# Performance work log

Measured on AMD Instinct MI355X. Metric: run time of the kernel, lower is better.

## Reference

```python
import jax, jax.numpy as jnp
import numpy as np

ALPHA = 0.2  # leaky_relu negative slope
NEG_INF = -9e15


def gat_layer(h_in, W, a, adj_mask):
    """One GATLayer (eval mode, dropout disabled).
    h_in: [N, F_in], W: [F_in, F_out], a: [2*F_out, 1], adj_mask: [N, N] bool.
    Equivalent to the torch repeat/cat construction: e_ij = leaky_relu(a1.h_i + a2.h_j).
    """
    h = h_in @ W                          # [N, F_out]
    F_out = W.shape[1]
    a1 = a[:F_out, 0]                     # [F_out]
    a2 = a[F_out:, 0]                     # [F_out]
    f1 = h @ a1                           # [N]
    f2 = h @ a2                           # [N]
    e = jax.nn.leaky_relu(f1[:, None] + f2[None, :], negative_slope=ALPHA)  # [N, N]
    e = jnp.where(adj_mask, e, NEG_INF)
    attn = jax.nn.softmax(e, axis=-1)     # rows sum to 1
    return jax.nn.elu(attn @ h)           # [N, F_out]


def setup_inputs() -> dict:
    key = jax.random.key(0)
    ks = jax.random.split(key, 6)
    N, F_in, F_hid, F_out, H = 8192, 29, 8, 2, 4
    x = jax.random.normal(ks[0], (N, F_in), dtype=jnp.float32)
    adj = jax.random.randint(ks[1], (N, N), 0, 2, dtype=jnp.int32)
    # xavier_uniform with gain=1.414
    def xavier(k, shape, gain=1.414):
        fan_in, fan_out = shape[0], shape[1]
        bound = gain * np.sqrt(6.0 / (fan_in + fan_out))
        return jax.random.uniform(k, shape, jnp.float32, -bound, bound)
    W_heads = jnp.stack([xavier(k, (F_in, F_hid)) for k in jax.random.split(ks[2], H)])   # [H, 29, 8]
    a_heads = jnp.stack([xavier(k, (2 * F_hid, 1)) for k in jax.random.split(ks[3], H)])  # [H, 16, 1]
    W_out = xavier(ks[4], (F_hid * H, F_out))   # [32, 2]
    a_out = xavier(ks[5], (2 * F_out, 1))       # [4, 1]
    return {"x": x, "adj": adj, "W_heads": W_heads, "a_heads": a_heads,
            "W_out": W_out, "a_out": a_out}


def reference(x, adj, W_heads, a_heads, W_out, a_out):
    adj_mask = adj > 0
    heads = jax.vmap(lambda W, a: gat_layer(x, W, a, adj_mask))(W_heads, a_heads)  # [H, N, 8]
    hcat = jnp.concatenate(list(heads), axis=1)   # [N, H*8] (same order as torch cat over heads)
    out = gat_layer(hcat, W_out, a_out, adj_mask)  # [N, 2]
    return jax.nn.log_softmax(out, axis=1)
```

## Files before the change

kernel.cpp:

```cpp
#include <hip/hip_runtime.h>
#include <math.h>

#define N 8192
#define NW 128
#define FIN 29
#define FH 8
#define NH 4
#define ALPHA 0.2f
#define LOG2E 1.4426950408889634f

typedef unsigned long long ull;

__device__ inline unsigned bf16rn(float f) {
    unsigned u = __float_as_uint(f);
    return (u + 0x7fffu + ((u >> 16) & 1u)) >> 16;
}
__device__ inline float2 bfpair(unsigned u) {
    return make_float2(__uint_as_float(u << 16), __uint_as_float(u & 0xffff0000u));
}
__device__ inline unsigned fenc(float x) {
    unsigned u = __float_as_uint(x);
    return (u & 0x80000000u) ? ~u : (u | 0x80000000u);
}
__device__ inline float fdec(unsigned e) {
    return __uint_as_float((e & 0x80000000u) ? (e & 0x7fffffffu) : ~e);
}

__global__ void k0_pack(const int* __restrict__ adj, ull* __restrict__ mask,
                        unsigned* __restrict__ amax) {
    int row = blockIdx.x;
    int tid = threadIdx.x;
    int lane = tid & 63;
    int wave = tid >> 6;
    if (row == 0 && tid < 8) amax[tid] = 0u;
    const int* rp = adj + (size_t)row * N;
#pragma unroll 8
    for (int i = 0; i < 32; i++) {
        int a = rp[i * 256 + tid];
        ull b = __ballot(a > 0);
        if (lane == 0) mask[(size_t)row * NW + i * 4 + wave] = b;
    }
}

__global__ __launch_bounds__(64) void k1_feat(
    const float* __restrict__ x, const float* __restrict__ Wh,
    const float* __restrict__ ah,
    float* __restrict__ f2p, uint4* __restrict__ hpk,
    float* __restrict__ f1a, unsigned* __restrict__ amax) {
    __shared__ float sW[NH * FIN * FH];
    __shared__ float sa[NH * 2 * FH];
    int tid = threadIdx.x;
    for (int i = tid; i < NH * FIN * FH; i += 64) sW[i] = Wh[i];
    for (int i = tid; i < NH * 2 * FH; i += 64) sa[i] = ah[i];
    __syncthreads();
    int node = blockIdx.x * 64 + tid;
    float xr[FIN];
#pragma unroll
    for (int f = 0; f < FIN; f++) xr[f] = x[node * FIN + f];
    float f2v[NH];
#pragma unroll
    for (int h = 0; h < NH; h++) {
        float hv[FH];
#pragma unroll
        for (int k = 0; k < FH; k++) {
            float s = 0.f;
#pragma unroll
            for (int f = 0; f < FIN; f++) s += xr[f] * sW[(h * FIN + f) * FH + k];
            hv[k] = s;
        }
        float f1 = 0.f, f2 = 0.f;
#pragma unroll
        for (int k = 0; k < FH; k++) {
            f1 += hv[k] * sa[h * 16 + k];
            f2 += hv[k] * sa[h * 16 + 8 + k];
        }
        f2v[h] = f2 * LOG2E;
        f2p[h * N + node] = f2v[h];
        f1a[node * 4 + h] = f1 * LOG2E;
        uint4 p;
        p.x = (bf16rn(hv[1]) << 16) | bf16rn(hv[0]);
        p.y = (bf16rn(hv[3]) << 16) | bf16rn(hv[2]);
        p.z = (bf16rn(hv[5]) << 16) | bf16rn(hv[4]);
        p.w = (bf16rn(hv[7]) << 16) | bf16rn(hv[6]);
        hpk[h * N + node] = p;
    }
#pragma unroll
    for (int h = 0; h < NH; h++) {
        float v = f2v[h];
        for (int off = 32; off > 0; off >>= 1) v = fmaxf(v, __shfl_xor(v, off, 64));
        if (tid == 0) atomicMax(&amax[h], fenc(v));
    }
}

#define TJ 512
#define JS1 2
__global__ __launch_bounds__(512) void k3_attn1(
    const ull* __restrict__ mask, const float* __restrict__ f2p,
    const uint4* __restrict__ hpk, const float* __restrict__ f1a,
    const unsigned* __restrict__ amax, float* __restrict__ part1) {
    __shared__ float tF2[TJ];
    __shared__ uint4 tH[TJ];
    int tid = threadIdx.x;
    int lane = tid & 63;
    int wave = tid >> 6;
    int h = blockIdx.x & 3;
    int js = (blockIdx.x >> 2) & (JS1 - 1);
    int rowblk = blockIdx.x >> 3;
    int r0 = rowblk * 16 + wave * 2;
    int r1 = r0 + 1;
    const int JR = N / JS1;
    int jbase = js * JR;

    float mf = fdec(amax[h]);
    float f1 = f1a[r0 * 4 + h];
    float v = f1 + mf, m = fmaxf(v, ALPHA * v);
    float f1m0 = f1 - m, f1q0 = ALPHA * f1 - m;
    f1 = f1a[r1 * 4 + h];
    v = f1 + mf; m = fmaxf(v, ALPHA * v);
    float f1m1 = f1 - m, f1q1 = ALPHA * f1 - m;

    float acc0[FH], acc1[FH], d0 = 0.f, d1 = 0.f;
#pragma unroll
    for (int k = 0; k < FH; k++) { acc0[k] = 0.f; acc1[k] = 0.f; }

    const ull* mr0 = mask + (size_t)r0 * NW;
    const ull* mr1 = mask + (size_t)r1 * NW;

    for (int t = 0; t < JR / TJ; t++) {
        __syncthreads();
        int gb = jbase + t * TJ + tid;
        tH[tid] = hpk[h * N + gb];
        tF2[tid] = f2p[h * N + gb];
        __syncthreads();
        int wb = (jbase >> 6) + t * (TJ / 64);
#pragma unroll
        for (int s = 0; s < TJ / 64; s++) {
            ull mw0 = mr0[wb + s];
            ull mw1 = mr1[wb + s];
            bool b0 = (mw0 >> lane) & 1ull;
            bool b1 = (mw1 >> lane) & 1ull;
            int jl = s * 64 + lane;
            float f2 = tF2[jl];
            uint4 hq = tH[jl];
            float2 hv01 = bfpair(hq.x);
            float2 hv23 = bfpair(hq.y);
            float2 hv45 = bfpair(hq.z);
            float2 hv67 = bfpair(hq.w);
            float p = ALPHA * f2;
            float w0 = __builtin_amdgcn_exp2f(fmaxf(f1m0 + f2, p + f1q0));
            w0 = b0 ? w0 : 0.f;
            float w1 = __builtin_amdgcn_exp2f(fmaxf(f1m1 + f2, p + f1q1));
            w1 = b1 ? w1 : 0.f;
            acc0[0] = fmaf(w0, hv01.x, acc0[0]);
            acc0[1] = fmaf(w0, hv01.y, acc0[1]);
            acc0[2] = fmaf(w0, hv23.x, acc0[2]);
            acc0[3] = fmaf(w0, hv23.y, acc0[3]);
            acc0[4] = fmaf(w0, hv45.x, acc0[4]);
            acc0[5] = fmaf(w0, hv45.y, acc0[5]);
            acc0[6] = fmaf(w0, hv67.x, acc0[6]);
            acc0[7] = fmaf(w0, hv67.y, acc0[7]);
            d0 += w0;
            acc1[0] = fmaf(w1, hv01.x, acc1[0]);
            acc1[1] = fmaf(w1, hv01.y, acc1[1]);
            acc1[2] = fmaf(w1, hv23.x, acc1[2]);
            acc1[3] = fmaf(w1, hv23.y, acc1[3]);
            acc1[4] = fmaf(w1, hv45.x, acc1[4]);
            acc1[5] = fmaf(w1, hv45.y, acc1[5]);
            acc1[6] = fmaf(w1, hv67.x, acc1[6]);
            acc1[7] = fmaf(w1, hv67.y, acc1[7]);
            d1 += w1;
        }
    }
#pragma unroll
    for (int k = 0; k < FH; k++) {
        for (int off = 32; off > 0; off >>= 1) {
            acc0[k] += __shfl_xor(acc0[k], off, 64);
            acc1[k] += __shfl_xor(acc1[k], off, 64);
        }
    }
    for (int off = 32; off > 0; off >>= 1) {
        d0 += __shfl_xor(d0, off, 64);
        d1 += __shfl_xor(d1, off, 64);
    }
    if (lane == 0) {
#pragma unroll
        for (int k = 0; k < FH; k++) {
            part1[(js * 36 + h * 9 + k) * N + r0] = acc0[k];
            part1[(js * 36 + h * 9 + k) * N + r1] = acc1[k];
        }
        part1[(js * 36 + h * 9 + 8) * N + r0] = d0;
        part1[(js * 36 + h * 9 + 8) * N + r1] = d1;
    }
}

__global__ void k3b_final(const float* __restrict__ part1, const float* __restrict__ Wo,
                          const float* __restrict__ ao,
                          float4* __restrict__ rec2, float* __restrict__ f1b,
                          unsigned* __restrict__ amax) {
    __shared__ float sW[64];
    __shared__ float sa[4];
    int tid = threadIdx.x;
    if (tid < 64) sW[tid] = Wo[tid];
    if (tid < 4) sa[tid] = ao[tid];
    __syncthreads();
    int row = blockIdx.x * 256 + tid;
    float hv[32];
#pragma unroll
    for (int h = 0; h < NH; h++) {
        float s[9];
#pragma unroll
        for (int c = 0; c < 9; c++)
            s[c] = part1[(h * 9 + c) * N + row] + part1[(36 + h * 9 + c) * N + row];
        float inv = 1.f / s[8];
#pragma unroll
        for (int k = 0; k < FH; k++) {
            float o = s[k] * inv;
            hv[h * 8 + k] = (o > 0.f) ? o : expm1f(o);
        }
    }
    float h0 = 0.f, h1 = 0.f;
#pragma unroll
    for (int i = 0; i < 32; i++) {
        h0 = fmaf(hv[i], sW[i * 2 + 0], h0);
        h1 = fmaf(hv[i], sW[i * 2 + 1], h1);
    }
    float f1 = (h0 * sa[0] + h1 * sa[1]) * LOG2E;
    float f2 = (h0 * sa[2] + h1 * sa[3]) * LOG2E;
    rec2[row] = make_float4(f2, h0, h1, 0.f);
    f1b[row] = f1;
    float vmax = f2;
    for (int off = 32; off > 0; off >>= 1) vmax = fmaxf(vmax, __shfl_xor(vmax, off, 64));
    if ((tid & 63) == 0) atomicMax(&amax[4], fenc(vmax));
}

#define JS2 4
__global__ __launch_bounds__(256) void k6_attn2(
    const ull* __restrict__ mask, const float4* __restrict__ rec2,
    const float* __restrict__ f1b, const unsigned* __restrict__ amax,
    float* __restrict__ part2) {
    int tid = threadIdx.x;
    int lane = tid & 63;
    int wave = tid >> 6;
    int blk = blockIdx.x >> 2;
    int js = blockIdx.x & 3;
    int rbase = blk * 16 + wave * 4;
    const int JR = N / JS2;
    int jbase = js * JR;

    float mb = fdec(amax[4]);
    float f1m[4], f1q[4];
#pragma unroll
    for (int i = 0; i < 4; i++) {
        float f1 = f1b[rbase + i];
        float v = f1 + mb, m = fmaxf(v, ALPHA * v);
        f1m[i] = f1 - m; f1q[i] = ALPHA * f1 - m;
    }
    float a0[4] = {0.f, 0.f, 0.f, 0.f};
    float a1[4] = {0.f, 0.f, 0.f, 0.f};
    float dd[4] = {0.f, 0.f, 0.f, 0.f};
    const ull* mr[4];
#pragma unroll
    for (int i = 0; i < 4; i++) mr[i] = mask + (size_t)(rbase + i) * NW;

    int wb = jbase >> 6;
#pragma unroll 4
    for (int s = 0; s < JR / 64; s++) {
        float4 q = rec2[jbase + s * 64 + lane];
        float p = ALPHA * q.x;
#pragma unroll
        for (int i = 0; i < 4; i++) {
            ull mw = mr[i][wb + s];
            float w = __builtin_amdgcn_exp2f(fmaxf(f1m[i] + q.x, p + f1q[i]));
            w = ((mw >> lane) & 1ull) ? w : 0.f;
            a0[i] = fmaf(w, q.y, a0[i]);
            a1[i] = fmaf(w, q.z, a1[i]);
            dd[i] += w;
        }
    }
#pragma unroll
    for (int i = 0; i < 4; i++) {
        for (int off = 32; off > 0; off >>= 1) {
            a0[i] += __shfl_xor(a0[i], off, 64);
            a1[i] += __shfl_xor(a1[i], off, 64);
            dd[i] += __shfl_xor(dd[i], off, 64);
        }
    }
    if (lane == 0) {
#pragma unroll
        for (int i = 0; i < 4; i++) {
            int row = rbase + i;
            part2[(js * 3 + 0) * N + row] = a0[i];
            part2[(js * 3 + 1) * N + row] = a1[i];
            part2[(js * 3 + 2) * N + row] = dd[i];
        }
    }
}

__global__ void k6b_final(const float* __restrict__ part2, float* __restrict__ out) {
    int row = blockIdx.x * 256 + threadIdx.x;
    float s0 = 0.f, s1 = 0.f, d = 0.f;
#pragma unroll
    for (int js = 0; js < JS2; js++) {
        s0 += part2[(js * 3 + 0) * N + row];
        s1 += part2[(js * 3 + 1) * N + row];
        d  += part2[(js * 3 + 2) * N + row];
    }
    float inv = 1.f / d;
    float e0 = s0 * inv, e1 = s1 * inv;
    e0 = (e0 > 0.f) ? e0 : expm1f(e0);
    e1 = (e1 > 0.f) ? e1 : expm1f(e1);
    float mx = fmaxf(e0, e1);
    float lse = mx + logf(expf(e0 - mx) + expf(e1 - mx));
    ((float2*)out)[row] = make_float2(e0 - lse, e1 - lse);
}

extern "C" void kernel_launch(void* const* d_in, const int* in_sizes, int n_in,
                              void* d_out, int out_size, void* d_ws, size_t ws_size,
                              hipStream_t stream) {
    const float* x   = (const float*)d_in[0];
    const int*   adj = (const int*)d_in[1];
    const float* Wh  = (const float*)d_in[2];
    const float* ah  = (const float*)d_in[3];
    const float* Wo  = (const float*)d_in[4];
    const float* ao  = (const float*)d_in[5];
    float* out = (float*)d_out;
    float* ws = (float*)d_ws;

    ull*      mask  = (ull*)ws;
    float*    f2p   = ws + 2097152;
    uint4*    hpk   = (uint4*)(ws + 2129920);
    float*    f1a   = ws + 2260992;
    float*    part1 = ws + 2293760;
    float4*   rec2  = (float4*)(ws + 2883584);
    float*    f1b   = ws + 2916352;
    float*    part2 = ws + 2924544;
    unsigned* amax  = (unsigned*)(ws + 3022848);

    k0_pack<<<N, 256, 0, stream>>>(adj, mask, amax);
    k1_feat<<<N / 64, 64, 0, stream>>>(x, Wh, ah, f2p, hpk, f1a, amax);
    k3_attn1<<<(N / 16) * JS1 * NH, 512, 0, stream>>>(mask, f2p, hpk, f1a, amax, part1);
    k3b_final<<<N / 256, 256, 0, stream>>>(part1, Wo, ao, rec2, f1b, amax);
    k6_attn2<<<(N / 16) * JS2, 256, 0, stream>>>(mask, rec2, f1b, amax, part2);
    k6b_final<<<N / 256, 256, 0, stream>>>(part2, out);
}
```

Baseline: 617.6 us.

## Compute first-layer attention aggregation with bf16 MFMA and factored exponentials

```diff
diff --git a/kernel.cpp b/kernel.cpp
--- a/kernel.cpp
+++ b/kernel.cpp
@@ -8,15 +8,18 @@
 #define NH 4
 #define ALPHA 0.2f
 #define LOG2E 1.4426950408889634f
+#define JS 4
+#define JRR (N / JS)
+#define JS2 4
 
 typedef unsigned long long ull;
+typedef unsigned short u16;
+typedef __attribute__((ext_vector_type(8))) short bf16x8;
+typedef __attribute__((ext_vector_type(4))) float f32x4;
 
 __device__ inline unsigned bf16rn(float f) {
     unsigned u = __float_as_uint(f);
     return (u + 0x7fffu + ((u >> 16) & 1u)) >> 16;
-}
-__device__ inline float2 bfpair(unsigned u) {
-    return make_float2(__uint_as_float(u << 16), __uint_as_float(u & 0xffff0000u));
 }
 __device__ inline unsigned fenc(float x) {
     unsigned u = __float_as_uint(x);
@@ -45,7 +48,7 @@
 __global__ __launch_bounds__(64) void k1_feat(
     const float* __restrict__ x, const float* __restrict__ Wh,
     const float* __restrict__ ah,
-    float* __restrict__ f2p, uint4* __restrict__ hpk,
+    float2* __restrict__ e2, u16* __restrict__ Ht,
     float* __restrict__ f1a, unsigned* __restrict__ amax) {
     __shared__ float sW[NH * FIN * FH];
     __shared__ float sa[NH * 2 * FH];
@@ -74,15 +77,15 @@
             f1 += hv[k] * sa[h * 16 + k];
             f2 += hv[k] * sa[h * 16 + 8 + k];
         }
-        f2v[h] = f2 * LOG2E;
-        f2p[h * N + node] = f2v[h];
-        f1a[node * 4 + h] = f1 * LOG2E;
-        uint4 p;
-        p.x = (bf16rn(hv[1]) << 16) | bf16rn(hv[0]);
-        p.y = (bf16rn(hv[3]) << 16) | bf16rn(hv[2]);
-        p.z = (bf16rn(hv[5]) << 16) | bf16rn(hv[4]);
-        p.w = (bf16rn(hv[7]) << 16) | bf16rn(hv[6]);
-        hpk[h * N + node] = p;
+        float f1L = f1 * LOG2E, f2L = f2 * LOG2E;
+        f2v[h] = f2L;
+        f1a[node * 4 + h] = f1L;
+        e2[h * N + node] = make_float2(__builtin_amdgcn_exp2f(f2L),
+                                       __builtin_amdgcn_exp2f(ALPHA * f2L));
+#pragma unroll
+        for (int k = 0; k < FH; k++)
+            Ht[(size_t)(h * 9 + k) * N + node] = (u16)bf16rn(hv[k]);
+        Ht[(size_t)(h * 9 + 8) * N + node] = 0x3F80u;
     }
 #pragma unroll
     for (int h = 0; h < NH; h++) {
@@ -92,104 +95,84 @@
     }
 }
 
-#define TJ 512
-#define JS1 2
-__global__ __launch_bounds__(512) void k3_attn1(
-    const ull* __restrict__ mask, const float* __restrict__ f2p,
-    const uint4* __restrict__ hpk, const float* __restrict__ f1a,
+__global__ __launch_bounds__(256) void k3_attn1(
+    const ull* __restrict__ mask, const float2* __restrict__ e2,
+    const u16* __restrict__ Ht, const float* __restrict__ f1a,
     const unsigned* __restrict__ amax, float* __restrict__ part1) {
-    __shared__ float tF2[TJ];
-    __shared__ uint4 tH[TJ];
+    __shared__ __align__(16) float2 sE2[JRR];
     int tid = threadIdx.x;
     int lane = tid & 63;
     int wave = tid >> 6;
     int h = blockIdx.x & 3;
-    int js = (blockIdx.x >> 2) & (JS1 - 1);
-    int rowblk = blockIdx.x >> 3;
-    int r0 = rowblk * 16 + wave * 2;
-    int r1 = r0 + 1;
-    const int JR = N / JS1;
-    int jbase = js * JR;
-
-    float mf = fdec(amax[h]);
-    float f1 = f1a[r0 * 4 + h];
-    float v = f1 + mf, m = fmaxf(v, ALPHA * v);
-    float f1m0 = f1 - m, f1q0 = ALPHA * f1 - m;
-    f1 = f1a[r1 * 4 + h];
-    v = f1 + mf; m = fmaxf(v, ALPHA * v);
-    float f1m1 = f1 - m, f1q1 = ALPHA * f1 - m;
-
-    float acc0[FH], acc1[FH], d0 = 0.f, d1 = 0.f;
-#pragma unroll
-    for (int k = 0; k < FH; k++) { acc0[k] = 0.f; acc1[k] = 0.f; }
-
-    const ull* mr0 = mask + (size_t)r0 * NW;
-    const ull* mr1 = mask + (size_t)r1 * NW;
-
-    for (int t = 0; t < JR / TJ; t++) {
-        __syncthreads();
-        int gb = jbase + t * TJ + tid;
-        tH[tid] = hpk[h * N + gb];
-        tF2[tid] = f2p[h * N + gb];
-        __syncthreads();
-        int wb = (jbase >> 6) + t * (TJ / 64);
-#pragma unroll
-        for (int s = 0; s < TJ / 64; s++) {
-            ull mw0 = mr0[wb + s];
-            ull mw1 = mr1[wb + s];
-            bool b0 = (mw0 >> lane) & 1ull;
-            bool b1 = (mw1 >> lane) & 1ull;
-            int jl = s * 64 + lane;
-            float f2 = tF2[jl];
-            uint4 hq = tH[jl];
-            float2 hv01 = bfpair(hq.x);
-            float2 hv23 = bfpair(hq.y);
-            float2 hv45 = bfpair(hq.z);
-            float2 hv67 = bfpair(hq.w);
-            float p = ALPHA * f2;
-            float w0 = __builtin_amdgcn_exp2f(fmaxf(f1m0 + f2, p + f1q0));
-            w0 = b0 ? w0 : 0.f;
-            float w1 = __builtin_amdgcn_exp2f(fmaxf(f1m1 + f2, p + f1q1));
-            w1 = b1 ? w1 : 0.f;
-            acc0[0] = fmaf(w0, hv01.x, acc0[0]);
-            acc0[1] = fmaf(w0, hv01.y, acc0[1]);
-            acc0[2] = fmaf(w0, hv23.x, acc0[2]);
-            acc0[3] = fmaf(w0, hv23.y, acc0[3]);
-            acc0[4] = fmaf(w0, hv45.x, acc0[4]);
-            acc0[5] = fmaf(w0, hv45.y, acc0[5]);
-            acc0[6] = fmaf(w0, hv67.x, acc0[6]);
-            acc0[7] = fmaf(w0, hv67.y, acc0[7]);
-            d0 += w0;
-            acc1[0] = fmaf(w1, hv01.x, acc1[0]);
-            acc1[1] = fmaf(w1, hv01.y, acc1[1]);
-            acc1[2] = fmaf(w1, hv23.x, acc1[2]);
-            acc1[3] = fmaf(w1, hv23.y, acc1[3]);
-            acc1[4] = fmaf(w1, hv45.x, acc1[4]);
-            acc1[5] = fmaf(w1, hv45.y, acc1[5]);
-            acc1[6] = fmaf(w1, hv67.x, acc1[6]);
-            acc1[7] = fmaf(w1, hv67.y, acc1[7]);
-            d1 += w1;
-        }
-    }
-#pragma unroll
-    for (int k = 0; k < FH; k++) {
-        for (int off = 32; off > 0; off >>= 1) {
-            acc0[k] += __shfl_xor(acc0[k], off, 64);
-            acc1[k] += __shfl_xor(acc1[k], off, 64);
-        }
-    }
-    for (int off = 32; off > 0; off >>= 1) {
-        d0 += __shfl_xor(d0, off, 64);
-        d1 += __shfl_xor(d1, off, 64);
-    }
-    if (lane == 0) {
-#pragma unroll
-        for (int k = 0; k < FH; k++) {
-            part1[(js * 36 + h * 9 + k) * N + r0] = acc0[k];
-            part1[(js * 36 + h * 9 + k) * N + r1] = acc1[k];
-        }
-        part1[(js * 36 + h * 9 + 8) * N + r0] = d0;
-        part1[(js * 36 + h * 9 + 8) * N + r1] = d1;
+    int js = (blockIdx.x >> 2) & 3;
+    int rowblk = blockIdx.x >> 4;
+    int jbase = js * JRR;
+
+    {
+        const float4* src = (const float4*)(e2 + (size_t)h * N + jbase);
+        float4* dst = (float4*)sE2;
+#pragma unroll
+        for (int i = 0; i < (JRR / 2) / 256; i++)
+            dst[tid + i * 256] = src[tid + i * 256];
+    }
+
+    int c = lane & 15;
+    int kb = lane >> 4;
+    int sh = kb * 8;
+    int r = rowblk * 64 + wave * 16 + c;
+
+    float mfL = fdec(amax[h]);
+    float f1 = f1a[r * 4 + h];
+    float v = f1 + mfL, m = fmaxf(v, ALPHA * v);
+    float e1p = __builtin_amdgcn_exp2f(f1 - m);
+    float e1n = __builtin_amdgcn_exp2f(ALPHA * f1 - m);
+
+    const ull* mrow = mask + (size_t)r * NW + (jbase >> 6);
+    const char* bbase = (const char*)(Ht + ((size_t)(h * 9 + c) * N + jbase + kb * 8));
+
+    f32x4 acc = {0.f, 0.f, 0.f, 0.f};
+    __syncthreads();
+
+    for (int t = 0; t < JRR / 64; t++) {
+        ull mw = mrow[t];
+        unsigned mlo = (unsigned)mw;
+        unsigned mhi = (unsigned)(mw >> 32);
+#pragma unroll
+        for (int hf = 0; hf < 2; hf++) {
+            unsigned sw = (hf ? mhi : mlo) >> sh;
+            const float4* qp = (const float4*)(sE2 + t * 64 + hf * 32 + kb * 8);
+            float4 q0 = qp[0], q1 = qp[1], q2 = qp[2], q3 = qp[3];
+            float w0 = fmaxf(e1p * q0.x, e1n * q0.y);
+            float w1 = fmaxf(e1p * q0.z, e1n * q0.w);
+            float w2 = fmaxf(e1p * q1.x, e1n * q1.y);
+            float w3 = fmaxf(e1p * q1.z, e1n * q1.w);
+            float w4 = fmaxf(e1p * q2.x, e1n * q2.y);
+            float w5 = fmaxf(e1p * q2.z, e1n * q2.w);
+            float w6 = fmaxf(e1p * q3.x, e1n * q3.y);
+            float w7 = fmaxf(e1p * q3.z, e1n * q3.w);
+            w0 = (sw & 1u)   ? w0 : 0.f;
+            w1 = (sw & 2u)   ? w1 : 0.f;
+            w2 = (sw & 4u)   ? w2 : 0.f;
+            w3 = (sw & 8u)   ? w3 : 0.f;
+            w4 = (sw & 16u)  ? w4 : 0.f;
+            w5 = (sw & 32u)  ? w5 : 0.f;
+            w6 = (sw & 64u)  ? w6 : 0.f;
+            w7 = (sw & 128u) ? w7 : 0.f;
+            uint4 ap;
+            asm("v_cvt_pk_bf16_f32 %0, %1, %2" : "=v"(ap.x) : "v"(w0), "v"(w1));
+            asm("v_cvt_pk_bf16_f32 %0, %1, %2" : "=v"(ap.y) : "v"(w2), "v"(w3));
+            asm("v_cvt_pk_bf16_f32 %0, %1, %2" : "=v"(ap.z) : "v"(w4), "v"(w5));
+            asm("v_cvt_pk_bf16_f32 %0, %1, %2" : "=v"(ap.w) : "v"(w6), "v"(w7));
+            uint4 bp = *(const uint4*)(bbase + t * 128 + hf * 64);
+            acc = __builtin_amdgcn_mfma_f32_16x16x32_bf16(
+                __builtin_bit_cast(bf16x8, ap), __builtin_bit_cast(bf16x8, bp),
+                acc, 0, 0, 0);
+        }
+    }
+    if (c <= 8) {
+        int rowout = rowblk * 64 + wave * 16 + kb * 4;
+        float* dst = part1 + (size_t)(js * 36 + h * 9 + c) * N + rowout;
+        *(float4*)dst = make_float4(acc[0], acc[1], acc[2], acc[3]);
     }
 }
 
@@ -209,8 +192,13 @@
     for (int h = 0; h < NH; h++) {
         float s[9];
 #pragma unroll
-        for (int c = 0; c < 9; c++)
-            s[c] = part1[(h * 9 + c) * N + row] + part1[(36 + h * 9 + c) * N + row];
+        for (int cc = 0; cc < 9; cc++) {
+            float acc = 0.f;
+#pragma unroll
+            for (int js = 0; js < JS; js++)
+                acc += part1[(size_t)(js * 36 + h * 9 + cc) * N + row];
+            s[cc] = acc;
+        }
         float inv = 1.f / s[8];
 #pragma unroll
         for (int k = 0; k < FH; k++) {
@@ -226,14 +214,14 @@
     }
     float f1 = (h0 * sa[0] + h1 * sa[1]) * LOG2E;
     float f2 = (h0 * sa[2] + h1 * sa[3]) * LOG2E;
-    rec2[row] = make_float4(f2, h0, h1, 0.f);
+    rec2[row] = make_float4(__builtin_amdgcn_exp2f(f2), h0, h1,
+                            __builtin_amdgcn_exp2f(ALPHA * f2));
     f1b[row] = f1;
     float vmax = f2;
     for (int off = 32; off > 0; off >>= 1) vmax = fmaxf(vmax, __shfl_xor(vmax, off, 64));
     if ((tid & 63) == 0) atomicMax(&amax[4], fenc(vmax));
 }
 
-#define JS2 4
 __global__ __launch_bounds__(256) void k6_attn2(
     const ull* __restrict__ mask, const float4* __restrict__ rec2,
     const float* __restrict__ f1b, const unsigned* __restrict__ amax,
@@ -248,12 +236,13 @@
     int jbase = js * JR;
 
     float mb = fdec(amax[4]);
-    float f1m[4], f1q[4];
+    float e1p[4], e1n[4];
 #pragma unroll
     for (int i = 0; i < 4; i++) {
         float f1 = f1b[rbase + i];
         float v = f1 + mb, m = fmaxf(v, ALPHA * v);
-        f1m[i] = f1 - m; f1q[i] = ALPHA * f1 - m;
+        e1p[i] = __builtin_amdgcn_exp2f(f1 - m);
+        e1n[i] = __builtin_amdgcn_exp2f(ALPHA * f1 - m);
     }
     float a0[4] = {0.f, 0.f, 0.f, 0.f};
     float a1[4] = {0.f, 0.f, 0.f, 0.f};
@@ -266,11 +255,10 @@
 #pragma unroll 4
     for (int s = 0; s < JR / 64; s++) {
         float4 q = rec2[jbase + s * 64 + lane];
-        float p = ALPHA * q.x;
 #pragma unroll
         for (int i = 0; i < 4; i++) {
             ull mw = mr[i][wb + s];
-            float w = __builtin_amdgcn_exp2f(fmaxf(f1m[i] + q.x, p + f1q[i]));
+            float w = fmaxf(e1p[i] * q.x, e1n[i] * q.w);
             w = ((mw >> lane) & 1ull) ? w : 0.f;
             a0[i] = fmaf(w, q.y, a0[i]);
             a1[i] = fmaf(w, q.z, a1[i]);
@@ -327,18 +315,18 @@
     float* ws = (float*)d_ws;
 
     ull*      mask  = (ull*)ws;
-    float*    f2p   = ws + 2097152;
-    uint4*    hpk   = (uint4*)(ws + 2129920);
-    float*    f1a   = ws + 2260992;
-    float*    part1 = ws + 2293760;
-    float4*   rec2  = (float4*)(ws + 2883584);
-    float*    f1b   = ws + 2916352;
-    float*    part2 = ws + 2924544;
-    unsigned* amax  = (unsigned*)(ws + 3022848);
+    float2*   e2    = (float2*)(ws + 2097152);
+    u16*      Ht    = (u16*)(ws + 2162688);
+    float*    f1a   = ws + 2310144;
+    float*    part1 = ws + 2342912;
+    float4*   rec2  = (float4*)(ws + 3522560);
+    float*    f1b   = ws + 3555328;
+    float*    part2 = ws + 3563520;
+    unsigned* amax  = (unsigned*)(ws + 3661824);
 
     k0_pack<<<N, 256, 0, stream>>>(adj, mask, amax);
-    k1_feat<<<N / 64, 64, 0, stream>>>(x, Wh, ah, f2p, hpk, f1a, amax);
-    k3_attn1<<<(N / 16) * JS1 * NH, 512, 0, stream>>>(mask, f2p, hpk, f1a, amax, part1);
+    k1_feat<<<N / 64, 64, 0, stream>>>(x, Wh, ah, e2, Ht, f1a, amax);
+    k3_attn1<<<(N / 64) * JS * NH, 256, 0, stream>>>(mask, e2, Ht, f1a, amax, part1);
     k3b_final<<<N / 256, 256, 0, stream>>>(part1, Wo, ao, rec2, f1b, amax);
     k6_attn2<<<(N / 16) * JS2, 256, 0, stream>>>(mask, rec2, f1b, amax, part2);
     k6b_final<<<N / 256, 256, 0, stream>>>(part2, out);
```

After: 531.6 us. 1.16x faster.
